# Kernel optimization log

Measured on AMD Instinct MI355X. Metric: run time of the kernel, lower is better.

## Reference

```python
import jax, jax.numpy as jnp
import numpy as np

B, C, OC, H, W = 2, 64, 128, 96, 96
HD, DI, N, R, K = C // 2, C, 16, 2, 4  # VSSBlock: hidden=C/2, d_inner=2*hidden=C, d_state, dt_rank, 4 scan dirs
EPS = 1e-5


def _conv(x, w, b, pad, groups=1):
    y = jax.lax.conv_general_dilated(x, w, (1, 1), pad, feature_group_count=groups,
                                     dimension_numbers=('NCHW', 'OIHW', 'NCHW'))
    return y + b[None, :, None, None]


def _ln(x, w, b):
    m = x.mean(-1, keepdims=True)
    v = x.var(-1, keepdims=True)
    return (x - m) * jax.lax.rsqrt(v + EPS) * w + b


def _selective_scan(xs, dts, Bs, Cs, A, D):
    # xs, dts: (B,K,DI,L); Bs, Cs: (B,K,N,L); A: (K,DI,N); D: (K,DI)
    dts = jax.nn.softplus(dts)

    def step(h, inp):
        u_t, dt_t, B_t, C_t = inp
        dA = jnp.exp(dt_t[..., None] * A)                         # (B,K,DI,N)
        h = dA * h + (dt_t * u_t)[..., None] * B_t[:, :, None, :]
        return h, jnp.einsum('bkdn,bkn->bkd', h, C_t)

    seq = (jnp.moveaxis(xs, -1, 0), jnp.moveaxis(dts, -1, 0),
           jnp.moveaxis(Bs, -1, 0), jnp.moveaxis(Cs, -1, 0))
    h0 = jnp.zeros(xs.shape[:3] + (A.shape[-1],), xs.dtype)
    _, ys = jax.lax.scan(step, h0, seq)
    return jnp.moveaxis(ys, 0, -1) + D[None, :, :, None] * xs


def _vss_block(x, ln_w, ln_b, in_w, conv_w, conv_b, xproj_w, dtproj_w, dtproj_b,
               A_logs, Ds, on_w, on_b, out_w):
    # x: (B,H,W,HD); VMamba SS2D with 4-direction cross-scan + residual
    b, hh, ww, _ = x.shape
    L = hh * ww
    h = _ln(x, ln_w, ln_b)
    xz = h @ in_w                                   # (B,H,W,2*DI)
    xp, z = jnp.split(xz, 2, axis=-1)
    xc = jnp.transpose(xp, (0, 3, 1, 2))            # (B,DI,H,W)
    xc = jax.nn.silu(_conv(xc, conv_w, conv_b, ((1, 1), (1, 1)), groups=DI))
    x_flat = xc.reshape(b, DI, L)
    x_wh = jnp.transpose(xc, (0, 1, 3, 2)).reshape(b, DI, L)
    x2 = jnp.stack([x_flat, x_wh], axis=1)
    xs = jnp.concatenate([x2, jnp.flip(x2, -1)], axis=1)      # (B,4,DI,L)
    x_dbl = jnp.einsum('bkdl,kcd->bkcl', xs, xproj_w)
    dts, Bs, Cs = jnp.split(x_dbl, [R, R + N], axis=2)
    dts = jnp.einsum('bkrl,kdr->bkdl', dts, dtproj_w) + dtproj_b[None, :, :, None]
    A = -jnp.exp(A_logs)
    ys = _selective_scan(xs, dts, Bs, Cs, A, Ds)              # (B,4,DI,L)
    inv = jnp.flip(ys[:, 2:4], -1)
    unwh = lambda t: jnp.transpose(t.reshape(b, DI, ww, hh), (0, 1, 3, 2)).reshape(b, DI, L)
    y = ys[:, 0] + inv[:, 0] + unwh(ys[:, 1]) + unwh(inv[:, 1])
    y = jnp.transpose(y.reshape(b, DI, hh, ww), (0, 2, 3, 1))
    y = _ln(y, on_w, on_b) * jax.nn.silu(z)
    return x + y @ out_w


def _forward(x, ms_dw33_w, ms_dw33_b, ms_in_w, ms_in_b, ms_scale,
             vss_ln_w, vss_ln_b, vss_in_w, vss_conv_w, vss_conv_b, vss_xproj_w,
             vss_dtproj_w, vss_dtproj_b, vss_A_logs, vss_Ds, vss_on_w, vss_on_b, vss_out_w,
             ma_conv_w, ma_conv_b, adw_h_w, adw_h_b, adw_w_w, adw_w_b,
             pw_w, pw_b, bn_w, bn_b, bn_mean, bn_var):
    vss = (vss_ln_w, vss_ln_b, vss_in_w, vss_conv_w, vss_conv_b, vss_xproj_w,
           vss_dtproj_w, vss_dtproj_b, vss_A_logs, vss_Ds, vss_on_w, vss_on_b, vss_out_w)
    # --- MambaSplit (shared VSSBlock applied to both channel halves) ---
    xd = _conv(x, ms_dw33_w, ms_dw33_b, ((1, 1), (1, 1)), groups=C)
    x1, x2 = jnp.split(xd, 2, axis=1)

    def branch(xp):
        y = _vss_block(jnp.transpose(xp, (0, 2, 3, 1)), *vss)
        return ms_scale * xp + jnp.transpose(y, (0, 3, 1, 2))

    xm = jnp.concatenate([branch(x1), branch(x2)], axis=1)
    m = xm.mean((2, 3), keepdims=True)
    v = xm.var((2, 3), keepdims=True)
    xm = (xm - m) * jax.lax.rsqrt(v + EPS) * ms_in_w[None, :, None, None] + ms_in_b[None, :, None, None]
    xm = jax.nn.leaky_relu(xm, 0.01)
    # --- MaxAvg (global avg+max pool -> 3x3 conv on 1x1 map -> sigmoid gate) ---
    pooled = jnp.concatenate([x.mean((2, 3), keepdims=True), x.max((2, 3), keepdims=True)], axis=1)
    gate = jax.nn.sigmoid(_conv(pooled, ma_conv_w, ma_conv_b, ((1, 1), (1, 1))))
    xs_ = xm + gate * x
    # --- AxialDW ---
    xs_ = xs_ + _conv(xs_, adw_h_w, adw_h_b, ((1, 1), (0, 0)), groups=C) \
              + _conv(xs_, adw_w_w, adw_w_b, ((0, 0), (1, 1)), groups=C)
    # --- BN (eval) + ReLU, 1x1 conv, 2x2 maxpool ---
    skip = jax.nn.relu((xs_ - bn_mean[None, :, None, None]) * jax.lax.rsqrt(bn_var[None, :, None, None] + EPS)
                       * bn_w[None, :, None, None] + bn_b[None, :, None, None])
    out = _conv(skip, pw_w, pw_b, ((0, 0), (0, 0)))
    down = jax.lax.reduce_window(out, -jnp.inf, jax.lax.max, (1, 1, 2, 2), (1, 1, 2, 2), 'VALID')
    return down, skip


def setup_inputs() -> dict:
    key = jax.random.key(0)
    ks = jax.random.split(key, 16)
    r = lambda i, shape, s=0.02: jax.random.normal(ks[i], shape, jnp.float32) * s
    return {
        'x': jax.random.normal(ks[0], (B, C, H, W), jnp.float32),
        'ms_dw33_w': r(1, (C, 1, 3, 3), 0.1), 'ms_dw33_b': jnp.zeros(C),
        'ms_in_w': jnp.ones(C), 'ms_in_b': jnp.zeros(C),
        'ms_scale': jnp.ones((1,)),
        'vss_ln_w': jnp.ones(HD), 'vss_ln_b': jnp.zeros(HD),
        'vss_in_w': r(2, (HD, 2 * DI)),
        'vss_conv_w': r(3, (DI, 1, 3, 3), 0.1), 'vss_conv_b': jnp.zeros(DI),
        'vss_xproj_w': r(4, (K, R + 2 * N, DI)),
        'vss_dtproj_w': r(5, (K, DI, R), 0.1), 'vss_dtproj_b': r(6, (K, DI), 0.1),
        'vss_A_logs': jnp.tile(jnp.log(jnp.arange(1, N + 1, dtype=jnp.float32)), (K, DI, 1)),
        'vss_Ds': jnp.ones((K, DI)),
        'vss_on_w': jnp.ones(DI), 'vss_on_b': jnp.zeros(DI),
        'vss_out_w': r(7, (DI, HD)),
        'ma_conv_w': r(8, (C, 2 * C, 3, 3), 0.05), 'ma_conv_b': jnp.zeros(C),
        'adw_h_w': r(9, (C, 1, 3, 1), 0.1), 'adw_h_b': jnp.zeros(C),
        'adw_w_w': r(10, (C, 1, 1, 3), 0.1), 'adw_w_b': jnp.zeros(C),
        'pw_w': r(11, (OC, C, 1, 1)), 'pw_b': jnp.zeros(OC),
        'bn_w': jnp.ones(C), 'bn_b': jnp.zeros(C),
        'bn_mean': jnp.zeros(C), 'bn_var': jnp.ones(C),
    }


def reference(x, ms_dw33_w, ms_dw33_b, ms_in_w, ms_in_b, ms_scale,
              vss_ln_w, vss_ln_b, vss_in_w, vss_conv_w, vss_conv_b, vss_xproj_w,
              vss_dtproj_w, vss_dtproj_b, vss_A_logs, vss_Ds, vss_on_w, vss_on_b, vss_out_w,
              ma_conv_w, ma_conv_b, adw_h_w, adw_h_b, adw_w_w, adw_w_b,
              pw_w, pw_b, bn_w, bn_b, bn_mean, bn_var):
    return _forward(x, ms_dw33_w, ms_dw33_b, ms_in_w, ms_in_b, ms_scale,
                    vss_ln_w, vss_ln_b, vss_in_w, vss_conv_w, vss_conv_b, vss_xproj_w,
                    vss_dtproj_w, vss_dtproj_b, vss_A_logs, vss_Ds, vss_on_w, vss_on_b, vss_out_w,
                    ma_conv_w, ma_conv_b, adw_h_w, adw_h_b, adw_w_w, adw_w_b,
                    pw_w, pw_b, bn_w, bn_b, bn_mean, bn_var)
```

## Files before the change

kernel.cpp:

```cpp
#include <hip/hip_runtime.h>
#include <hip/hip_bf16.h>

typedef __hip_bfloat16 bf16;
#define DEV __device__ __forceinline__

constexpr int B_ = 2, C_ = 64, H_ = 96, W_ = 96, L_ = 9216;
constexpr int HD_ = 32, DI_ = 64, N_ = 16, K_ = 4, BB_ = 4;
constexpr int OC_ = 128;
constexpr int CH_ = 384, CL_ = 24;
constexpr float EPSF = 1e-5f;
constexpr int DOWN_SZ = B_ * OC_ * 48 * 48;

typedef __attribute__((ext_vector_type(8))) short short8;
typedef __attribute__((ext_vector_type(4))) float f32x4;

DEV float softplusf(float x) { return x > 15.f ? x : __logf(1.f + __expf(x)); }
DEV float b2f(bf16 v) { return __bfloat162float(v); }
DEV float lo16f(unsigned v) { return __uint_as_float(v << 16); }
DEV float hi16f(unsigned v) { return __uint_as_float(v & 0xffff0000u); }
DEV void unpk(uint4 a, uint4 b, float* v) {
  v[0] = lo16f(a.x); v[1] = hi16f(a.x); v[2] = lo16f(a.y); v[3] = hi16f(a.y);
  v[4] = lo16f(a.z); v[5] = hi16f(a.z); v[6] = lo16f(a.w); v[7] = hi16f(a.w);
  v[8] = lo16f(b.x); v[9] = hi16f(b.x); v[10] = lo16f(b.y); v[11] = hi16f(b.y);
  v[12] = lo16f(b.z); v[13] = hi16f(b.z); v[14] = lo16f(b.w); v[15] = hi16f(b.w);
}

__constant__ float kLogN[16] = {
  0.0f, 0.69314718f, 1.09861229f, 1.38629436f, 1.60943791f, 1.79175947f,
  1.94591015f, 2.07944154f, 2.19722458f, 2.30258509f, 2.39789527f,
  2.48490665f, 2.56494936f, 2.63905733f, 2.70805020f, 2.77258872f};

DEV void chunk_addr(int k, int chunk, int& idx0, int& stride) {
  int r4 = chunk & 3, q = chunk >> 2;
  if (k == 0)      { idx0 = chunk * CL_;                        stride = 1;   }
  else if (k == 1) { idx0 = (24 * r4) * 96 + q;                 stride = 96;  }
  else if (k == 2) { idx0 = L_ - 1 - chunk * CL_;               stride = -1;  }
  else             { idx0 = (95 - 24 * r4) * 96 + (95 - q);     stride = -96; }
}

DEV void pow_tree(float e1, float* ep) {
  float e2 = e1 * e1, e4 = e2 * e2, e8 = e4 * e4;
  float e3 = e2 * e1, e5 = e4 * e1, e6 = e4 * e2, e7 = e4 * e3;
  ep[0] = e1;  ep[1] = e2;  ep[2] = e3;  ep[3] = e4;
  ep[4] = e5;  ep[5] = e6;  ep[6] = e7;  ep[7] = e8;
  ep[8] = e8 * e1;  ep[9] = e8 * e2;  ep[10] = e8 * e3;  ep[11] = e8 * e4;
  ep[12] = e8 * e5; ep[13] = e8 * e6; ep[14] = e8 * e7;  ep[15] = e8 * e8;
}

DEV void ldrow(const float* __restrict__ bB, const bf16* __restrict__ bC,
               const bf16* __restrict__ xcb, int d, int idx,
               uint4& qb0, uint4& qb1, uint4& qc0, uint4& qc1,
               float& t0, float& t1, float& u) {
  int uix = __builtin_amdgcn_readfirstlane(idx);
  const float* p = bB + (size_t)uix * 12;
  qb0 = *(const uint4*)p; qb1 = *(const uint4*)(p + 4);
  t0 = p[8]; t1 = p[9];
  const uint4* cq = (const uint4*)(bC + (size_t)uix * 16);
  qc0 = cq[0]; qc1 = cq[1];
  u = b2f(xcb[(size_t)idx * DI_ + d]);
}

DEV void pstep(uint4 qb0, uint4 qb1, uint4 qc0, uint4 qc1, float t0, float t1, float u,
               float w0, float w1, float bia, float A1, float Dk,
               float* h, float& S, float& yout) {
  float Bv[16], Cv[16];
  unpk(qb0, qb1, Bv); unpk(qc0, qc1, Cv);
  float dt = softplusf(fmaf(t0, w0, fmaf(t1, w1, bia)));
  S += dt;
  float du = dt * u;
  float ep[16];
  pow_tree(__expf(dt * A1), ep);
  float m[16];
#pragma unroll
  for (int n = 0; n < N_; n++) {
    h[n] = fmaf(ep[n], h[n], du * Bv[n]);
    m[n] = h[n] * Cv[n];
  }
  float a0 = m[0] + m[1], a1 = m[2] + m[3], a2 = m[4] + m[5], a3 = m[6] + m[7];
  float a4 = m[8] + m[9], a5 = m[10] + m[11], a6 = m[12] + m[13], a7 = m[14] + m[15];
  float b0 = a0 + a1, b1 = a2 + a3, b2 = a4 + a5, b3 = a6 + a7;
  yout = fmaf(Dk, u, (b0 + b1) + (b2 + b3));
}

__global__ void k_dw33(const float* __restrict__ x, const float* __restrict__ w,
                       const float* __restrict__ bias, float* __restrict__ out) {
  int t = blockIdx.x * 256 + threadIdx.x;
  if (t >= B_ * C_ * L_) return;
  int wi = t % W_, hi = (t / W_) % H_, c = (t / L_) % C_;
  float acc = bias[c];
#pragma unroll
  for (int dy = -1; dy <= 1; dy++) {
    int hh = hi + dy; if (hh < 0 || hh >= H_) continue;
#pragma unroll
    for (int dx = -1; dx <= 1; dx++) {
      int ww = wi + dx; if (ww < 0 || ww >= W_) continue;
      acc = fmaf(x[t + dy * W_ + dx], w[c * 9 + (dy + 1) * 3 + (dx + 1)], acc);
    }
  }
  out[t] = acc;
}

__global__ __launch_bounds__(256, 4) void k_ln_inproj(
    const float* __restrict__ xd, const float* __restrict__ lnw,
    const float* __restrict__ lnb, const float* __restrict__ inw,
    float* __restrict__ xzA, bf16* __restrict__ xzBh) {
  int bb = blockIdx.y, t = threadIdx.x;
  int b = bb & 1, co = (bb >> 1) * HD_;
  int idx0 = blockIdx.x * 64;
  __shared__ float xds[32 * 68];
  __shared__ float meanA[64], rstdA[64];
  int lane = t & 63;
  for (int r = 0; r < 8; r++) {
    int c = r * 4 + (t >> 6);
    xds[c * 68 + lane] = xd[(size_t)(b * C_ + co + c) * L_ + idx0 + lane];
  }
  __syncthreads();
  if (t < 64) {
    float s = 0.f, sq = 0.f;
#pragma unroll
    for (int c = 0; c < 32; c++) { float v = xds[c * 68 + t]; s += v; sq = fmaf(v, v, sq); }
    float mean = s * (1.f / HD_);
    float var = sq * (1.f / HD_) - mean * mean;
    meanA[t] = mean; rstdA[t] = rsqrtf(var + EPSF);
  }
  __syncthreads();
  for (int i = t; i < 2048; i += 256) {
    int c = i >> 6, idx = i & 63;
    float v = xds[c * 68 + idx];
    xds[c * 68 + idx] = (v - meanA[idx]) * rstdA[idx] * lnw[c] + lnb[c];
  }
  __syncthreads();
  int oc = t & 127, g = t >> 7;
  float acc[32];
#pragma unroll
  for (int j = 0; j < 32; j++) acc[j] = 0.f;
  for (int c = 0; c < 32; c++) {
    float wv = inw[c * 128 + oc];
    const float4* row = reinterpret_cast<const float4*>(&xds[c * 68 + g * 32]);
#pragma unroll
    for (int j4 = 0; j4 < 8; j4++) {
      float4 xv = row[j4];
      acc[j4 * 4 + 0] = fmaf(xv.x, wv, acc[j4 * 4 + 0]);
      acc[j4 * 4 + 1] = fmaf(xv.y, wv, acc[j4 * 4 + 1]);
      acc[j4 * 4 + 2] = fmaf(xv.z, wv, acc[j4 * 4 + 2]);
      acc[j4 * 4 + 3] = fmaf(xv.w, wv, acc[j4 * 4 + 3]);
    }
  }
  int occ = oc & 63;
  if (oc < 64) {
#pragma unroll
    for (int j = 0; j < 32; j++)
      xzA[(size_t)(bb * L_ + idx0 + g * 32 + j) * 64 + occ] = acc[j];
  } else {
#pragma unroll
    for (int j = 0; j < 32; j++)
      xzBh[(size_t)(bb * L_ + idx0 + g * 32 + j) * 64 + occ] = __float2bfloat16(acc[j]);
  }
}

__global__ void k_dwsilu(const float* __restrict__ xzA, const float* __restrict__ cw,
                         const float* __restrict__ cb, bf16* __restrict__ xch) {
  int t = blockIdx.x * 256 + threadIdx.x;
  int d = t & 63, idx = (t >> 6) % L_, bb = t / (L_ * DI_);
  int wi = idx % W_, hi = idx / W_;
  float acc = cb[d];
#pragma unroll
  for (int dy = -1; dy <= 1; dy++) {
    int hh = hi + dy; if (hh < 0 || hh >= H_) continue;
#pragma unroll
    for (int dx = -1; dx <= 1; dx++) {
      int ww = wi + dx; if (ww < 0 || ww >= W_) continue;
      acc = fmaf(xzA[(size_t)(bb * L_ + hh * W_ + ww) * 64 + d],
                 cw[d * 9 + (dy + 1) * 3 + (dx + 1)], acc);
    }
  }
  acc = acc / (1.f + __expf(-acc));
  xch[t] = __float2bfloat16(acc);
}

__global__ void k_wprep(const float* __restrict__ xpw, const float* __restrict__ alog,
                        bf16* __restrict__ wh, float* __restrict__ aux) {
  int i = blockIdx.x * 256 + threadIdx.x;
  if (i < 144 * 64) {
    int n = i >> 6;
    wh[i] = __float2bfloat16(n < 136 ? xpw[i] : 0.f);
  }
  if (blockIdx.x == 0 && threadIdx.x < 256) {
    int kd = threadIdx.x;
    const float* al = alog + kd * N_;
    float a0 = al[0];
    bool lin = true;
#pragma unroll
    for (int n = 1; n < N_; n++) lin = lin && (fabsf(al[n] - a0 - kLogN[n]) < 3e-5f);
    aux[kd] = -__expf(a0);
    aux[256 + kd] = lin ? 1.f : 0.f;
#pragma unroll
    for (int n = 0; n < N_; n++) aux[512 + kd * N_ + n] = -__expf(al[n]);
  }
}

__global__ __launch_bounds__(256, 4) void k_xdbl_mfma(
    const bf16* __restrict__ xch, const bf16* __restrict__ wh,
    float* __restrict__ xdblB, bf16* __restrict__ xdblC) {
  int w = threadIdx.x >> 6, lane = threadIdx.x & 63;
  int bb = blockIdx.y;
  int mtile = blockIdx.x * 4 + w;
  int idx0 = mtile * 16;
  int m = lane & 15, quad = lane >> 4;
  const bf16* arow = xch + ((size_t)bb * L_ + idx0 + m) * 64 + quad * 8;
  short8 a0 = *reinterpret_cast<const short8*>(arow);
  short8 a1 = *reinterpret_cast<const short8*>(arow + 32);
#pragma unroll
  for (int nt = 0; nt < 9; nt++) {
    int n = nt * 16 + m;
    const bf16* brow = wh + n * 64 + quad * 8;
    short8 b0 = *reinterpret_cast<const short8*>(brow);
    short8 b1 = *reinterpret_cast<const short8*>(brow + 32);
    f32x4 acc = {0.f, 0.f, 0.f, 0.f};
    acc = __builtin_amdgcn_mfma_f32_16x16x32_bf16(a0, b0, acc, 0, 0, 0);
    acc = __builtin_amdgcn_mfma_f32_16x16x32_bf16(a1, b1, acc, 0, 0, 0);
    if (n < 136) {
      int k4 = (n >= 102) ? 3 : (n >= 68) ? 2 : (n >= 34) ? 1 : 0;
      int c = n - k4 * 34;
      size_t row = (size_t)(bb * K_ + k4) * L_ + idx0 + quad * 4;
      if (c < 2) {
        float* db = xdblB + row * 12 + 8 + c;
        db[0] = acc[0]; db[12] = acc[1]; db[24] = acc[2]; db[36] = acc[3];
      } else if (c < 18) {
        bf16* bp = (bf16*)(xdblB + row * 12) + (c - 2);
        bp[0] = __float2bfloat16(acc[0]);  bp[24] = __float2bfloat16(acc[1]);
        bp[48] = __float2bfloat16(acc[2]); bp[72] = __float2bfloat16(acc[3]);
      } else {
        bf16* cp = xdblC + row * 16 + (c - 18);
        cp[0] = __float2bfloat16(acc[0]);  cp[16] = __float2bfloat16(acc[1]);
        cp[32] = __float2bfloat16(acc[2]); cp[48] = __float2bfloat16(acc[3]);
      }
    }
  }
}

__global__ __launch_bounds__(256, 4) void k_scan1(
    const float* __restrict__ xdblB, const bf16* __restrict__ xdblC,
    const bf16* __restrict__ xch, const float* __restrict__ dtw,
    const float* __restrict__ dtb, const float* __restrict__ Dsw,
    const float* __restrict__ aux, bf16* __restrict__ hbuf,
    float* __restrict__ ssum, bf16* __restrict__ ylocal, bf16* __restrict__ cdt) {
  int w = threadIdx.x >> 6, d = threadIdx.x & 63;
  int chunk = blockIdx.x * 4 + w, k = blockIdx.y, bb = blockIdx.z;
  float w0 = dtw[(k * DI_ + d) * 2 + 0], w1 = dtw[(k * DI_ + d) * 2 + 1];
  float bia = dtb[k * DI_ + d];
  float Dk = Dsw[k * DI_ + d];
  float A1 = aux[k * 64 + d];
  bool chain = (__ballot(aux[256 + k * 64 + d] > 0.5f) == ~0ull);
  float h[N_];
#pragma unroll
  for (int n = 0; n < N_; n++) h[n] = 0.f;
  int idx0, stride;
  chunk_addr(k, chunk, idx0, stride);
  const float* bB = xdblB + (size_t)(bb * K_ + k) * L_ * 12;
  const bf16* bC = xdblC + (size_t)(bb * K_ + k) * L_ * 16;
  const bf16* xcb = xch + (size_t)bb * L_ * DI_;
  bf16* yb = ylocal + (size_t)(bb * K_ + k) * L_ * DI_;
  bf16* cb2 = cdt + (size_t)(bb * K_ + k) * L_ * DI_;
  float S = 0.f;
  if (chain) {
    uint4 qb0a, qb1a, qc0a, qc1a; float t0a, t1a, ua;
    uint4 qb0b, qb1b, qc0b, qc1b; float t0b, t1b, ub;
    int ia = idx0;
    ldrow(bB, bC, xcb, d, ia, qb0a, qb1a, qc0a, qc1a, t0a, t1a, ua);
    for (int s = 0; s < CL_; s += 2) {
      int ib = ia + stride;
      ldrow(bB, bC, xcb, d, ib, qb0b, qb1b, qc0b, qc1b, t0b, t1b, ub);
      float y;
      pstep(qb0a, qb1a, qc0a, qc1a, t0a, t1a, ua, w0, w1, bia, A1, Dk, h, S, y);
      yb[(size_t)ia * DI_ + d] = __float2bfloat16(y);
      cb2[(size_t)ia * DI_ + d] = __float2bfloat16(S);
      int in2 = (s + 2 < CL_) ? ib + stride : idx0;
      ldrow(bB, bC, xcb, d, in2, qb0a, qb1a, qc0a, qc1a, t0a, t1a, ua);
      pstep(qb0b, qb1b, qc0b, qc1b, t0b, t1b, ub, w0, w1, bia, A1, Dk, h, S, y);
      yb[(size_t)ib * DI_ + d] = __float2bfloat16(y);
      cb2[(size_t)ib * DI_ + d] = __float2bfloat16(S);
      ia = in2;
    }
  } else {
    float A[N_];
#pragma unroll
    for (int n = 0; n < N_; n++) A[n] = aux[512 + (k * 64 + d) * N_ + n];
    int idx = idx0;
    for (int s = 0; s < CL_; s++) {
      uint4 qb0, qb1, qc0, qc1; float t0, t1, u;
      ldrow(bB, bC, xcb, d, idx, qb0, qb1, qc0, qc1, t0, t1, u);
      float Bv[16], Cv[16];
      unpk(qb0, qb1, Bv); unpk(qc0, qc1, Cv);
      float dt = softplusf(fmaf(t0, w0, fmaf(t1, w1, bia)));
      S += dt;
      float du = dt * u;
      float y = 0.f;
#pragma unroll
      for (int n = 0; n < N_; n++) {
        h[n] = fmaf(__expf(dt * A[n]), h[n], du * Bv[n]);
        y = fmaf(h[n], Cv[n], y);
      }
      y = fmaf(Dk, u, y);
      yb[(size_t)idx * DI_ + d] = __float2bfloat16(y);
      cb2[(size_t)idx * DI_ + d] = __float2bfloat16(S);
      idx += stride;
    }
  }
  size_t base = (size_t)((bb * K_ + k) * CH_ + chunk) * DI_ + d;
  ssum[base] = S;
#pragma unroll
  for (int n = 0; n < N_; n++) hbuf[base * N_ + n] = __float2bfloat16(h[n]);
}

__global__ void k_scan2(const float* __restrict__ aux, const float* __restrict__ ssum,
                        bf16* __restrict__ hbuf) {
  int t = blockIdx.x * 256 + threadIdx.x;
  int n = t & 15, d = (t >> 4) & 63, kk = (t >> 10) & 3, bb = t >> 12;
  float A = aux[512 + (kk * 64 + d) * N_ + n];
  size_t row = (size_t)(bb * K_ + kk) * CH_ * DI_ + d;
  constexpr int U = 16;
  float Sb[U], hb[U];
#pragma unroll
  for (int j = 0; j < U; j++) {
    size_t sb = row + (size_t)j * DI_;
    Sb[j] = ssum[sb]; hb[j] = b2f(hbuf[sb * N_ + n]);
  }
  float hp = 0.f;
  for (int c = 0; c < CH_; c += U) {
    float S2[U], h2[U];
    if (c + U < CH_) {
#pragma unroll
      for (int j = 0; j < U; j++) {
        size_t sb = row + (size_t)(c + U + j) * DI_;
        S2[j] = ssum[sb]; h2[j] = b2f(hbuf[sb * N_ + n]);
      }
    } else {
#pragma unroll
      for (int j = 0; j < U; j++) { S2[j] = 0.f; h2[j] = 0.f; }
    }
#pragma unroll
    for (int j = 0; j < U; j++) {
      size_t sb = row + (size_t)(c + j) * DI_;
      float e = __expf(A * Sb[j]);
      hbuf[sb * N_ + n] = __float2bfloat16(hp);
      hp = fmaf(e, hp, hb[j]);
    }
#pragma unroll
    for (int j = 0; j < U; j++) { Sb[j] = S2[j]; hb[j] = h2[j]; }
  }
}

__global__ __launch_bounds__(256, 4) void k_combine(
    const bf16* __restrict__ ylocal, const bf16* __restrict__ cdt,
    const bf16* __restrict__ hbuf, const bf16* __restrict__ xdblC,
    const float* __restrict__ aux, const bf16* __restrict__ xzBh,
    const float* __restrict__ xd, const float* __restrict__ onw,
    const float* __restrict__ onb, const float* __restrict__ outw,
    const float* __restrict__ mssc, float* __restrict__ xm) {
  int w = threadIdx.x >> 6, d = threadIdx.x & 63;
  int idx = blockIdx.x * 4 + w, bb = blockIdx.y;
  int b = bb & 1, co = (bb >> 1) * HD_;
  int hii = idx / 96, wii = idx - hii * 96;
  int lt = wii * 96 + hii;
  int lk[4] = { idx, lt, L_ - 1 - idx, L_ - 1 - lt };
  float y = 0.f;
#pragma unroll
  for (int k = 0; k < K_; k++) {
    int chunk = lk[k] / CL_;
    size_t row = (size_t)(bb * K_ + k) * L_ + idx;
    float yk = b2f(ylocal[row * DI_ + d]);
    float S = b2f(cdt[row * DI_ + d]);
    float A1 = aux[k * 64 + d];
    bool chain = (__ballot(aux[256 + k * 64 + d] > 0.5f) == ~0ull);
    const bf16* hb = hbuf + ((size_t)((bb * K_ + k) * CH_ + chunk) * DI_ + d) * N_;
    uint4 qh0 = *(const uint4*)hb, qh1 = *(const uint4*)(hb + 8);
    float hv[16];
    unpk(qh0, qh1, hv);
    const uint4* cq = (const uint4*)(xdblC + row * 16);
    float Cv[16];
    unpk(cq[0], cq[1], Cv);
    float corr;
    if (chain) {
      float ep[16];
      pow_tree(__expf(A1 * S), ep);
      float m[16];
#pragma unroll
      for (int n = 0; n < N_; n++) m[n] = Cv[n] * (ep[n] * hv[n]);
      float a0 = m[0] + m[1], a1 = m[2] + m[3], a2 = m[4] + m[5], a3 = m[6] + m[7];
      float a4 = m[8] + m[9], a5 = m[10] + m[11], a6 = m[12] + m[13], a7 = m[14] + m[15];
      corr = ((a0 + a1) + (a2 + a3)) + ((a4 + a5) + (a6 + a7));
    } else {
      corr = 0.f;
#pragma unroll
      for (int n = 0; n < N_; n++) {
        float A = aux[512 + (k * 64 + d) * N_ + n];
        corr = fmaf(Cv[n] * hv[n], __expf(A * S), corr);
      }
    }
    y += yk + corr;
  }
  float s = y, sq = y * y;
#pragma unroll
  for (int m = 1; m < 64; m <<= 1) { s += __shfl_xor(s, m, 64); sq += __shfl_xor(sq, m, 64); }
  float mean = s * (1.f / DI_);
  float var = sq * (1.f / DI_) - mean * mean;
  float rstd = rsqrtf(var + EPSF);
  float yn = (y - mean) * rstd * onw[d] + onb[d];
  float z = b2f(xzBh[(size_t)(bb * L_ + idx) * 64 + d]);
  float g = yn * (z / (1.f + __expf(-z)));
  __shared__ float gs[4][DI_];
  gs[w][d] = g;
  __syncthreads();
  if (d < HD_) {
    float acc = 0.f;
#pragma unroll
    for (int dd = 0; dd < DI_; dd++) acc = fmaf(gs[w][dd], outw[dd * HD_ + d], acc);
    size_t xi = (size_t)(b * C_ + co + d) * L_ + idx;
    float xp = xd[xi];
    xm[xi] = mssc[0] * xp + xp + acc;
  }
}

__global__ __launch_bounds__(1024) void k_stats(
    const float* __restrict__ xm, const float* __restrict__ x,
    float* __restrict__ inm, float* __restrict__ inr,
    float* __restrict__ xmean, float* __restrict__ xmax) {
  int bc = blockIdx.x, t = threadIdx.x;
  const float* pm = xm + (size_t)bc * L_;
  const float* px = x + (size_t)bc * L_;
  float s = 0.f, sq = 0.f, xs = 0.f, mx = -1e30f;
  for (int i = t; i < L_; i += 1024) {
    float v = pm[i]; s += v; sq = fmaf(v, v, sq);
    float xv = px[i]; xs += xv; mx = fmaxf(mx, xv);
  }
  __shared__ float red[64];
#pragma unroll
  for (int m = 1; m < 64; m <<= 1) {
    s += __shfl_xor(s, m, 64); sq += __shfl_xor(sq, m, 64);
    xs += __shfl_xor(xs, m, 64); mx = fmaxf(mx, __shfl_xor(mx, m, 64));
  }
  int wid = t >> 6;
  if ((t & 63) == 0) { red[wid] = s; red[16 + wid] = sq; red[32 + wid] = xs; red[48 + wid] = mx; }
  __syncthreads();
  if (t == 0) {
    s = 0.f; sq = 0.f; xs = 0.f; mx = -1e30f;
#pragma unroll
    for (int i = 0; i < 16; i++) {
      s += red[i]; sq += red[16 + i]; xs += red[32 + i]; mx = fmaxf(mx, red[48 + i]);
    }
    float mean = s * (1.f / L_);
    float var = sq * (1.f / L_) - mean * mean;
    inm[bc] = mean;
    inr[bc] = rsqrtf(var + EPSF);
    xmean[bc] = xs * (1.f / L_);
    xmax[bc] = mx;
  }
}

__global__ void k_xs(const float* __restrict__ xm, const float* __restrict__ inm,
                     const float* __restrict__ inr, const float* __restrict__ msw,
                     const float* __restrict__ msb, const float* __restrict__ xmean,
                     const float* __restrict__ xmax, const float* __restrict__ maw,
                     const float* __restrict__ mab, const float* __restrict__ x,
                     float* __restrict__ xs2) {
  int t = blockIdx.x * 256 + threadIdx.x;
  int bc = t / L_, c = bc & 63, b = bc >> 6;
  __shared__ float gsh;
  if (threadIdx.x < 64) {
    int ic = threadIdx.x;
    float p = xmean[b * 64 + ic] * maw[(c * 128 + ic) * 9 + 4]
            + xmax[b * 64 + ic] * maw[(c * 128 + 64 + ic) * 9 + 4];
#pragma unroll
    for (int m = 1; m < 64; m <<= 1) p += __shfl_xor(p, m, 64);
    if (ic == 0) gsh = 1.f / (1.f + __expf(-(p + mab[c])));
  }
  __syncthreads();
  float gate = gsh;
  float v = xm[t];
  v = (v - inm[bc]) * inr[bc] * msw[c] + msb[c];
  v = v > 0.f ? v : 0.01f * v;
  xs2[t] = v + gate * x[t];
}

__global__ void k_axbn(const float* __restrict__ xs2, const float* __restrict__ hw,
                       const float* __restrict__ hb, const float* __restrict__ wwt,
                       const float* __restrict__ wb, const float* __restrict__ bnw,
                       const float* __restrict__ bnb, const float* __restrict__ bnm,
                       const float* __restrict__ bnv, float* __restrict__ skipo) {
  int t = blockIdx.x * 256 + threadIdx.x;
  if (t >= B_ * C_ * L_) return;
  int wi = t % W_, hi = (t / W_) % H_, c = (t / L_) % C_;
  float a = xs2[t];
  float hacc = hb[c];
#pragma unroll
  for (int dy = -1; dy <= 1; dy++) {
    int hh = hi + dy; if (hh < 0 || hh >= H_) continue;
    hacc = fmaf(xs2[t + dy * W_], hw[c * 3 + dy + 1], hacc);
  }
  float wacc = wb[c];
#pragma unroll
  for (int dx = -1; dx <= 1; dx++) {
    int ww = wi + dx; if (ww < 0 || ww >= W_) continue;
    wacc = fmaf(xs2[t + dx], wwt[c * 3 + dx + 1], wacc);
  }
  float v = a + hacc + wacc;
  float sv = (v - bnm[c]) * rsqrtf(bnv[c] + EPSF) * bnw[c] + bnb[c];
  skipo[t] = fmaxf(sv, 0.f);
}

__global__ void k_pwpool(const float* __restrict__ skipo, const float* __restrict__ pww,
                         const float* __restrict__ pwb, float* __restrict__ down) {
  int h2 = blockIdx.x, b = blockIdx.y, t = threadIdx.x;
  int oc0 = blockIdx.z * 32;
  __shared__ float sk[64 * 192];
  for (int i = t; i < 64 * 192; i += 256) {
    int c = i / 192, rw = i % 192, r = rw / 96, wcol = rw % 96;
    sk[i] = skipo[((size_t)(b * C_ + c) * H_ + (2 * h2 + r)) * W_ + wcol];
  }
  __syncthreads();
  for (int o = t; o < 32 * 48; o += 256) {
    int oc = oc0 + o / 48, w2 = o % 48;
    float s0 = 0.f, s1 = 0.f, s2 = 0.f, s3 = 0.f;
#pragma unroll 8
    for (int c = 0; c < 64; c++) {
      float wv = pww[oc * 64 + c];
      const float* sp = &sk[c * 192 + 2 * w2];
      s0 = fmaf(sp[0], wv, s0);
      s1 = fmaf(sp[1], wv, s1);
      s2 = fmaf(sp[96], wv, s2);
      s3 = fmaf(sp[97], wv, s3);
    }
    float v = fmaxf(fmaxf(s0, s1), fmaxf(s2, s3)) + pwb[oc];
    down[((size_t)(b * OC_ + oc) * 48 + h2) * 48 + w2] = v;
  }
}

extern "C" void kernel_launch(void* const* d_in, const int* in_sizes, int n_in,
                              void* d_out, int out_size, void* d_ws, size_t ws_size,
                              hipStream_t stream) {
  const float* x     = (const float*)d_in[0];
  const float* dw33w = (const float*)d_in[1];
  const float* dw33b = (const float*)d_in[2];
  const float* msw   = (const float*)d_in[3];
  const float* msb   = (const float*)d_in[4];
  const float* mssc  = (const float*)d_in[5];
  const float* lnw   = (const float*)d_in[6];
  const float* lnb   = (const float*)d_in[7];
  const float* inw   = (const float*)d_in[8];
  const float* cw    = (const float*)d_in[9];
  const float* cb    = (const float*)d_in[10];
  const float* xpw   = (const float*)d_in[11];
  const float* dtw   = (const float*)d_in[12];
  const float* dtb   = (const float*)d_in[13];
  const float* alog  = (const float*)d_in[14];
  const float* Dsw   = (const float*)d_in[15];
  const float* onw   = (const float*)d_in[16];
  const float* onb   = (const float*)d_in[17];
  const float* outw  = (const float*)d_in[18];
  const float* maw   = (const float*)d_in[19];
  const float* mab   = (const float*)d_in[20];
  const float* ahw   = (const float*)d_in[21];
  const float* ahb   = (const float*)d_in[22];
  const float* aww   = (const float*)d_in[23];
  const float* awb   = (const float*)d_in[24];
  const float* pww   = (const float*)d_in[25];
  const float* pwb   = (const float*)d_in[26];
  const float* bnw   = (const float*)d_in[27];
  const float* bnb   = (const float*)d_in[28];
  const float* bnm   = (const float*)d_in[29];
  const float* bnv   = (const float*)d_in[30];

  float* ws = (float*)d_ws;
  float* xd    = ws;
  float* xzA   = xd + 1179648;
  bf16*  hbuf  = (bf16*)xzA;
  bf16*  xzBh  = (bf16*)(xzA + 3145728);
  float* xdblB = xzA + 3145728 + 1179648;
  bf16*  xdblC = (bf16*)(xdblB + 1769472);
  float* ssum  = xdblB + 1769472 + 1179648;
  bf16*  ylocal = (bf16*)(ssum + 393216);
  bf16*  cdt   = (bf16*)(ssum + 393216 + 4718592);
  float* xmR   = ssum + 393216 + 4718592 + 4718592;
  bf16*  xch   = (bf16*)xmR;
  float* xm    = xmR;
  float* xs2   = (float*)ylocal;
  float* st    = xmR + 1179648;
  float* inm = st, *inr = st + 128, *xmean = st + 256, *xmaxv = st + 384;
  float* aux   = st + 512;
  bf16*  wh    = (bf16*)(aux + 4608);

  float* outp = (float*)d_out;
  float* down = outp;
  float* skipo = outp + DOWN_SZ;

  dim3 b256(256);
  int nEl = B_ * C_ * L_;

  k_wprep<<<dim3(36), b256, 0, stream>>>(xpw, alog, wh, aux);
  k_dw33<<<dim3((nEl + 255) / 256), b256, 0, stream>>>(x, dw33w, dw33b, xd);
  k_ln_inproj<<<dim3(L_ / 64, BB_), b256, 0, stream>>>(xd, lnw, lnb, inw, xzA, xzBh);
  k_dwsilu<<<dim3(BB_ * L_ * DI_ / 256), b256, 0, stream>>>(xzA, cw, cb, xch);
  k_xdbl_mfma<<<dim3(L_ / 64, BB_), b256, 0, stream>>>(xch, wh, xdblB, xdblC);
  k_scan1<<<dim3(CH_ / 4, K_, BB_), b256, 0, stream>>>(xdblB, xdblC, xch, dtw, dtb, Dsw,
                                                       aux, hbuf, ssum, ylocal, cdt);
  k_scan2<<<dim3(BB_ * K_ * DI_ * N_ / 256), b256, 0, stream>>>(aux, ssum, hbuf);
  k_combine<<<dim3(L_ / 4, BB_), b256, 0, stream>>>(ylocal, cdt, hbuf, xdblC, aux, xzBh,
                                                    xd, onw, onb, outw, mssc, xm);
  k_stats<<<dim3(B_ * C_), dim3(1024), 0, stream>>>(xm, x, inm, inr, xmean, xmaxv);
  k_xs<<<dim3((nEl + 255) / 256), b256, 0, stream>>>(xm, inm, inr, msw, msb, xmean, xmaxv, maw, mab, x, xs2);
  k_axbn<<<dim3((nEl + 255) / 256), b256, 0, stream>>>(xs2, ahw, ahb, aww, awb, bnw, bnb, bnm, bnv, skipo);
  k_pwpool<<<dim3(48, B_, 4), b256, 0, stream>>>(skipo, pww, pwb, down);
}
```

Measured before the change: 333.0 us.

## Restructure chunked scan into three passes with carried-in states and halved chunk length

Replaces the two-pass chunked scan plus correction-in-combine with a three-pass scheme. Pass one computes only per-chunk end states and dt sums, pass two propagates chunk prefixes, and pass three re-runs each chunk from its true initial state to produce final outputs. The combine kernel then just sums the four directions. This drops the cumulative-dt buffer and the per-element correction work, and the chunk length is halved to 12 to double parallelism. The cost is reading B, u and dt twice, a longer sequential prefix pass over 768 chunks, and a larger state buffer.

```diff
diff --git a/kernel.cpp b/kernel.cpp
--- a/kernel.cpp
+++ b/kernel.cpp
@@ -7,7 +7,7 @@
 constexpr int B_ = 2, C_ = 64, H_ = 96, W_ = 96, L_ = 9216;
 constexpr int HD_ = 32, DI_ = 64, N_ = 16, K_ = 4, BB_ = 4;
 constexpr int OC_ = 128;
-constexpr int CH_ = 384, CL_ = 24;
+constexpr int CH_ = 768, CL_ = 12;
 constexpr float EPSF = 1e-5f;
 constexpr int DOWN_SZ = B_ * OC_ * 48 * 48;
 
@@ -31,11 +31,11 @@
   2.48490665f, 2.56494936f, 2.63905733f, 2.70805020f, 2.77258872f};
 
 DEV void chunk_addr(int k, int chunk, int& idx0, int& stride) {
-  int r4 = chunk & 3, q = chunk >> 2;
+  int r8 = chunk & 7, q = chunk >> 3;
   if (k == 0)      { idx0 = chunk * CL_;                        stride = 1;   }
-  else if (k == 1) { idx0 = (24 * r4) * 96 + q;                 stride = 96;  }
+  else if (k == 1) { idx0 = (12 * r8) * 96 + q;                 stride = 96;  }
   else if (k == 2) { idx0 = L_ - 1 - chunk * CL_;               stride = -1;  }
-  else             { idx0 = (95 - 24 * r4) * 96 + (95 - q);     stride = -96; }
+  else             { idx0 = (95 - 12 * r8) * 96 + (95 - q);     stride = -96; }
 }
 
 DEV void pow_tree(float e1, float* ep) {
@@ -47,10 +47,18 @@
   ep[12] = e8 * e5; ep[13] = e8 * e6; ep[14] = e8 * e7;  ep[15] = e8 * e8;
 }
 
-DEV void ldrow(const float* __restrict__ bB, const bf16* __restrict__ bC,
-               const bf16* __restrict__ xcb, int d, int idx,
-               uint4& qb0, uint4& qb1, uint4& qc0, uint4& qc1,
-               float& t0, float& t1, float& u) {
+DEV void ld_bu(const float* __restrict__ bB, const bf16* __restrict__ xcb, int d, int idx,
+               uint4& qb0, uint4& qb1, float& t0, float& t1, float& u) {
+  int uix = __builtin_amdgcn_readfirstlane(idx);
+  const float* p = bB + (size_t)uix * 12;
+  qb0 = *(const uint4*)p; qb1 = *(const uint4*)(p + 4);
+  t0 = p[8]; t1 = p[9];
+  u = b2f(xcb[(size_t)idx * DI_ + d]);
+}
+DEV void ld_bcu(const float* __restrict__ bB, const bf16* __restrict__ bC,
+                const bf16* __restrict__ xcb, int d, int idx,
+                uint4& qb0, uint4& qb1, uint4& qc0, uint4& qc1,
+                float& t0, float& t1, float& u) {
   int uix = __builtin_amdgcn_readfirstlane(idx);
   const float* p = bB + (size_t)uix * 12;
   qb0 = *(const uint4*)p; qb1 = *(const uint4*)(p + 4);
@@ -58,28 +66,6 @@
   const uint4* cq = (const uint4*)(bC + (size_t)uix * 16);
   qc0 = cq[0]; qc1 = cq[1];
   u = b2f(xcb[(size_t)idx * DI_ + d]);
-}
-
-DEV void pstep(uint4 qb0, uint4 qb1, uint4 qc0, uint4 qc1, float t0, float t1, float u,
-               float w0, float w1, float bia, float A1, float Dk,
-               float* h, float& S, float& yout) {
-  float Bv[16], Cv[16];
-  unpk(qb0, qb1, Bv); unpk(qc0, qc1, Cv);
-  float dt = softplusf(fmaf(t0, w0, fmaf(t1, w1, bia)));
-  S += dt;
-  float du = dt * u;
-  float ep[16];
-  pow_tree(__expf(dt * A1), ep);
-  float m[16];
-#pragma unroll
-  for (int n = 0; n < N_; n++) {
-    h[n] = fmaf(ep[n], h[n], du * Bv[n]);
-    m[n] = h[n] * Cv[n];
-  }
-  float a0 = m[0] + m[1], a1 = m[2] + m[3], a2 = m[4] + m[5], a3 = m[6] + m[7];
-  float a4 = m[8] + m[9], a5 = m[10] + m[11], a6 = m[12] + m[13], a7 = m[14] + m[15];
-  float b0 = a0 + a1, b1 = a2 + a3, b2 = a4 + a5, b3 = a6 + a7;
-  yout = fmaf(Dk, u, (b0 + b1) + (b2 + b3));
 }
 
 __global__ void k_dw33(const float* __restrict__ x, const float* __restrict__ w,
@@ -240,11 +226,109 @@
 }
 
 __global__ __launch_bounds__(256, 4) void k_scan1(
+    const float* __restrict__ xdblB, const bf16* __restrict__ xch,
+    const float* __restrict__ dtw, const float* __restrict__ dtb,
+    const float* __restrict__ aux, bf16* __restrict__ hbuf,
+    float* __restrict__ ssum) {
+  int w = threadIdx.x >> 6, d = threadIdx.x & 63;
+  int chunk = blockIdx.x * 4 + w, k = blockIdx.y, bb = blockIdx.z;
+  float w0 = dtw[(k * DI_ + d) * 2 + 0], w1 = dtw[(k * DI_ + d) * 2 + 1];
+  float bia = dtb[k * DI_ + d];
+  float A1 = aux[k * 64 + d];
+  bool chain = (__ballot(aux[256 + k * 64 + d] > 0.5f) == ~0ull);
+  float h[N_];
+#pragma unroll
+  for (int n = 0; n < N_; n++) h[n] = 0.f;
+  int idx0, stride;
+  chunk_addr(k, chunk, idx0, stride);
+  const float* bB = xdblB + (size_t)(bb * K_ + k) * L_ * 12;
+  const bf16* xcb = xch + (size_t)bb * L_ * DI_;
+  float S = 0.f;
+  if (chain) {
+    int idx = idx0;
+#pragma unroll 2
+    for (int s = 0; s < CL_; s++) {
+      uint4 qb0, qb1; float t0, t1, u;
+      ld_bu(bB, xcb, d, idx, qb0, qb1, t0, t1, u);
+      float Bv[16];
+      unpk(qb0, qb1, Bv);
+      float dt = softplusf(fmaf(t0, w0, fmaf(t1, w1, bia)));
+      S += dt;
+      float du = dt * u;
+      float ep[16];
+      pow_tree(__expf(dt * A1), ep);
+#pragma unroll
+      for (int n = 0; n < N_; n++) h[n] = fmaf(ep[n], h[n], du * Bv[n]);
+      idx += stride;
+    }
+  } else {
+    float A[N_];
+#pragma unroll
+    for (int n = 0; n < N_; n++) A[n] = aux[512 + (k * 64 + d) * N_ + n];
+    int idx = idx0;
+    for (int s = 0; s < CL_; s++) {
+      uint4 qb0, qb1; float t0, t1, u;
+      ld_bu(bB, xcb, d, idx, qb0, qb1, t0, t1, u);
+      float Bv[16];
+      unpk(qb0, qb1, Bv);
+      float dt = softplusf(fmaf(t0, w0, fmaf(t1, w1, bia)));
+      S += dt;
+      float du = dt * u;
+#pragma unroll
+      for (int n = 0; n < N_; n++) h[n] = fmaf(__expf(dt * A[n]), h[n], du * Bv[n]);
+      idx += stride;
+    }
+  }
+  size_t base = (size_t)((bb * K_ + k) * CH_ + chunk) * DI_ + d;
+  ssum[base] = S;
+#pragma unroll
+  for (int n = 0; n < N_; n++) hbuf[base * N_ + n] = __float2bfloat16(h[n]);
+}
+
+__global__ void k_scan2(const float* __restrict__ aux, const float* __restrict__ ssum,
+                        bf16* __restrict__ hbuf) {
+  int t = blockIdx.x * 256 + threadIdx.x;
+  int n = t & 15, d = (t >> 4) & 63, kk = (t >> 10) & 3, bb = t >> 12;
+  float A = aux[512 + (kk * 64 + d) * N_ + n];
+  size_t row = (size_t)(bb * K_ + kk) * CH_ * DI_ + d;
+  constexpr int U = 16;
+  float Sb[U], hb[U];
+#pragma unroll
+  for (int j = 0; j < U; j++) {
+    size_t sb = row + (size_t)j * DI_;
+    Sb[j] = ssum[sb]; hb[j] = b2f(hbuf[sb * N_ + n]);
+  }
+  float hp = 0.f;
+  for (int c = 0; c < CH_; c += U) {
+    float S2[U], h2[U];
+    if (c + U < CH_) {
+#pragma unroll
+      for (int j = 0; j < U; j++) {
+        size_t sb = row + (size_t)(c + U + j) * DI_;
+        S2[j] = ssum[sb]; h2[j] = b2f(hbuf[sb * N_ + n]);
+      }
+    } else {
+#pragma unroll
+      for (int j = 0; j < U; j++) { S2[j] = 0.f; h2[j] = 0.f; }
+    }
+#pragma unroll
+    for (int j = 0; j < U; j++) {
+      size_t sb = row + (size_t)(c + j) * DI_;
+      float e = __expf(A * Sb[j]);
+      hbuf[sb * N_ + n] = __float2bfloat16(hp);
+      hp = fmaf(e, hp, hb[j]);
+    }
+#pragma unroll
+    for (int j = 0; j < U; j++) { Sb[j] = S2[j]; hb[j] = h2[j]; }
+  }
+}
+
+__global__ __launch_bounds__(256, 4) void k_scan3(
     const float* __restrict__ xdblB, const bf16* __restrict__ xdblC,
     const bf16* __restrict__ xch, const float* __restrict__ dtw,
     const float* __restrict__ dtb, const float* __restrict__ Dsw,
-    const float* __restrict__ aux, bf16* __restrict__ hbuf,
-    float* __restrict__ ssum, bf16* __restrict__ ylocal, bf16* __restrict__ cdt) {
+    const float* __restrict__ aux, const bf16* __restrict__ hbuf,
+    bf16* __restrict__ ydir) {
   int w = threadIdx.x >> 6, d = threadIdx.x & 63;
   int chunk = blockIdx.x * 4 + w, k = blockIdx.y, bb = blockIdx.z;
   float w0 = dtw[(k * DI_ + d) * 2 + 0], w1 = dtw[(k * DI_ + d) * 2 + 1];
@@ -253,34 +337,42 @@
   float A1 = aux[k * 64 + d];
   bool chain = (__ballot(aux[256 + k * 64 + d] > 0.5f) == ~0ull);
   float h[N_];
-#pragma unroll
-  for (int n = 0; n < N_; n++) h[n] = 0.f;
+  size_t base = (size_t)((bb * K_ + k) * CH_ + chunk) * DI_ + d;
+  {
+    const bf16* hb = hbuf + base * N_;
+    uint4 qh0 = *(const uint4*)hb, qh1 = *(const uint4*)(hb + 8);
+    unpk(qh0, qh1, h);
+  }
   int idx0, stride;
   chunk_addr(k, chunk, idx0, stride);
   const float* bB = xdblB + (size_t)(bb * K_ + k) * L_ * 12;
   const bf16* bC = xdblC + (size_t)(bb * K_ + k) * L_ * 16;
   const bf16* xcb = xch + (size_t)bb * L_ * DI_;
-  bf16* yb = ylocal + (size_t)(bb * K_ + k) * L_ * DI_;
-  bf16* cb2 = cdt + (size_t)(bb * K_ + k) * L_ * DI_;
-  float S = 0.f;
+  bf16* yb = ydir + (size_t)(bb * K_ + k) * L_ * DI_;
   if (chain) {
-    uint4 qb0a, qb1a, qc0a, qc1a; float t0a, t1a, ua;
-    uint4 qb0b, qb1b, qc0b, qc1b; float t0b, t1b, ub;
-    int ia = idx0;
-    ldrow(bB, bC, xcb, d, ia, qb0a, qb1a, qc0a, qc1a, t0a, t1a, ua);
-    for (int s = 0; s < CL_; s += 2) {
-      int ib = ia + stride;
-      ldrow(bB, bC, xcb, d, ib, qb0b, qb1b, qc0b, qc1b, t0b, t1b, ub);
-      float y;
-      pstep(qb0a, qb1a, qc0a, qc1a, t0a, t1a, ua, w0, w1, bia, A1, Dk, h, S, y);
-      yb[(size_t)ia * DI_ + d] = __float2bfloat16(y);
-      cb2[(size_t)ia * DI_ + d] = __float2bfloat16(S);
-      int in2 = (s + 2 < CL_) ? ib + stride : idx0;
-      ldrow(bB, bC, xcb, d, in2, qb0a, qb1a, qc0a, qc1a, t0a, t1a, ua);
-      pstep(qb0b, qb1b, qc0b, qc1b, t0b, t1b, ub, w0, w1, bia, A1, Dk, h, S, y);
-      yb[(size_t)ib * DI_ + d] = __float2bfloat16(y);
-      cb2[(size_t)ib * DI_ + d] = __float2bfloat16(S);
-      ia = in2;
+    int idx = idx0;
+#pragma unroll 2
+    for (int s = 0; s < CL_; s++) {
+      uint4 qb0, qb1, qc0, qc1; float t0, t1, u;
+      ld_bcu(bB, bC, xcb, d, idx, qb0, qb1, qc0, qc1, t0, t1, u);
+      float Bv[16], Cv[16];
+      unpk(qb0, qb1, Bv); unpk(qc0, qc1, Cv);
+      float dt = softplusf(fmaf(t0, w0, fmaf(t1, w1, bia)));
+      float du = dt * u;
+      float ep[16];
+      pow_tree(__expf(dt * A1), ep);
+      float m[16];
+#pragma unroll
+      for (int n = 0; n < N_; n++) {
+        h[n] = fmaf(ep[n], h[n], du * Bv[n]);
+        m[n] = h[n] * Cv[n];
+      }
+      float a0 = m[0] + m[1], a1 = m[2] + m[3], a2 = m[4] + m[5], a3 = m[6] + m[7];
+      float a4 = m[8] + m[9], a5 = m[10] + m[11], a6 = m[12] + m[13], a7 = m[14] + m[15];
+      float b0 = a0 + a1, b1 = a2 + a3, b2 = a4 + a5, b3 = a6 + a7;
+      float y = fmaf(Dk, u, (b0 + b1) + (b2 + b3));
+      yb[(size_t)idx * DI_ + d] = __float2bfloat16(y);
+      idx += stride;
     }
   } else {
     float A[N_];
@@ -289,11 +381,10 @@
     int idx = idx0;
     for (int s = 0; s < CL_; s++) {
       uint4 qb0, qb1, qc0, qc1; float t0, t1, u;
-      ldrow(bB, bC, xcb, d, idx, qb0, qb1, qc0, qc1, t0, t1, u);
+      ld_bcu(bB, bC, xcb, d, idx, qb0, qb1, qc0, qc1, t0, t1, u);
       float Bv[16], Cv[16];
       unpk(qb0, qb1, Bv); unpk(qc0, qc1, Cv);
       float dt = softplusf(fmaf(t0, w0, fmaf(t1, w1, bia)));
-      S += dt;
       float du = dt * u;
       float y = 0.f;
 #pragma unroll
@@ -303,103 +394,22 @@
       }
       y = fmaf(Dk, u, y);
       yb[(size_t)idx * DI_ + d] = __float2bfloat16(y);
-      cb2[(size_t)idx * DI_ + d] = __float2bfloat16(S);
       idx += stride;
     }
   }
-  size_t base = (size_t)((bb * K_ + k) * CH_ + chunk) * DI_ + d;
-  ssum[base] = S;
-#pragma unroll
-  for (int n = 0; n < N_; n++) hbuf[base * N_ + n] = __float2bfloat16(h[n]);
-}
-
-__global__ void k_scan2(const float* __restrict__ aux, const float* __restrict__ ssum,
-                        bf16* __restrict__ hbuf) {
-  int t = blockIdx.x * 256 + threadIdx.x;
-  int n = t & 15, d = (t >> 4) & 63, kk = (t >> 10) & 3, bb = t >> 12;
-  float A = aux[512 + (kk * 64 + d) * N_ + n];
-  size_t row = (size_t)(bb * K_ + kk) * CH_ * DI_ + d;
-  constexpr int U = 16;
-  float Sb[U], hb[U];
-#pragma unroll
-  for (int j = 0; j < U; j++) {
-    size_t sb = row + (size_t)j * DI_;
-    Sb[j] = ssum[sb]; hb[j] = b2f(hbuf[sb * N_ + n]);
-  }
-  float hp = 0.f;
-  for (int c = 0; c < CH_; c += U) {
-    float S2[U], h2[U];
-    if (c + U < CH_) {
-#pragma unroll
-      for (int j = 0; j < U; j++) {
-        size_t sb = row + (size_t)(c + U + j) * DI_;
-        S2[j] = ssum[sb]; h2[j] = b2f(hbuf[sb * N_ + n]);
-      }
-    } else {
-#pragma unroll
-      for (int j = 0; j < U; j++) { S2[j] = 0.f; h2[j] = 0.f; }
-    }
-#pragma unroll
-    for (int j = 0; j < U; j++) {
-      size_t sb = row + (size_t)(c + j) * DI_;
-      float e = __expf(A * Sb[j]);
-      hbuf[sb * N_ + n] = __float2bfloat16(hp);
-      hp = fmaf(e, hp, hb[j]);
-    }
-#pragma unroll
-    for (int j = 0; j < U; j++) { Sb[j] = S2[j]; hb[j] = h2[j]; }
-  }
-}
-
-__global__ __launch_bounds__(256, 4) void k_combine(
-    const bf16* __restrict__ ylocal, const bf16* __restrict__ cdt,
-    const bf16* __restrict__ hbuf, const bf16* __restrict__ xdblC,
-    const float* __restrict__ aux, const bf16* __restrict__ xzBh,
-    const float* __restrict__ xd, const float* __restrict__ onw,
-    const float* __restrict__ onb, const float* __restrict__ outw,
-    const float* __restrict__ mssc, float* __restrict__ xm) {
+}
+
+__global__ void k_combine(const bf16* __restrict__ ydir, const bf16* __restrict__ xzBh,
+                          const float* __restrict__ xd, const float* __restrict__ onw,
+                          const float* __restrict__ onb, const float* __restrict__ outw,
+                          const float* __restrict__ mssc, float* __restrict__ xm) {
   int w = threadIdx.x >> 6, d = threadIdx.x & 63;
   int idx = blockIdx.x * 4 + w, bb = blockIdx.y;
   int b = bb & 1, co = (bb >> 1) * HD_;
-  int hii = idx / 96, wii = idx - hii * 96;
-  int lt = wii * 96 + hii;
-  int lk[4] = { idx, lt, L_ - 1 - idx, L_ - 1 - lt };
-  float y = 0.f;
-#pragma unroll
-  for (int k = 0; k < K_; k++) {
-    int chunk = lk[k] / CL_;
-    size_t row = (size_t)(bb * K_ + k) * L_ + idx;
-    float yk = b2f(ylocal[row * DI_ + d]);
-    float S = b2f(cdt[row * DI_ + d]);
-    float A1 = aux[k * 64 + d];
-    bool chain = (__ballot(aux[256 + k * 64 + d] > 0.5f) == ~0ull);
-    const bf16* hb = hbuf + ((size_t)((bb * K_ + k) * CH_ + chunk) * DI_ + d) * N_;
-    uint4 qh0 = *(const uint4*)hb, qh1 = *(const uint4*)(hb + 8);
-    float hv[16];
-    unpk(qh0, qh1, hv);
-    const uint4* cq = (const uint4*)(xdblC + row * 16);
-    float Cv[16];
-    unpk(cq[0], cq[1], Cv);
-    float corr;
-    if (chain) {
-      float ep[16];
-      pow_tree(__expf(A1 * S), ep);
-      float m[16];
-#pragma unroll
-      for (int n = 0; n < N_; n++) m[n] = Cv[n] * (ep[n] * hv[n]);
-      float a0 = m[0] + m[1], a1 = m[2] + m[3], a2 = m[4] + m[5], a3 = m[6] + m[7];
-      float a4 = m[8] + m[9], a5 = m[10] + m[11], a6 = m[12] + m[13], a7 = m[14] + m[15];
-      corr = ((a0 + a1) + (a2 + a3)) + ((a4 + a5) + (a6 + a7));
-    } else {
-      corr = 0.f;
-#pragma unroll
-      for (int n = 0; n < N_; n++) {
-        float A = aux[512 + (k * 64 + d) * N_ + n];
-        corr = fmaf(Cv[n] * hv[n], __expf(A * S), corr);
-      }
-    }
-    y += yk + corr;
-  }
+  const bf16* yd = ydir + (size_t)bb * K_ * L_ * DI_;
+  size_t off = (size_t)idx * DI_ + d;
+  float y = b2f(yd[off]) + b2f(yd[(size_t)L_ * DI_ + off])
+          + b2f(yd[(size_t)2 * L_ * DI_ + off]) + b2f(yd[(size_t)3 * L_ * DI_ + off]);
   float s = y, sq = y * y;
 #pragma unroll
   for (int m = 1; m < 64; m <<= 1) { s += __shfl_xor(s, m, 64); sq += __shfl_xor(sq, m, 64); }
@@ -573,18 +583,18 @@
 
   float* ws = (float*)d_ws;
   float* xd    = ws;
-  float* xzA   = xd + 1179648;
-  bf16*  hbuf  = (bf16*)xzA;
-  bf16*  xzBh  = (bf16*)(xzA + 3145728);
-  float* xdblB = xzA + 3145728 + 1179648;
+  float* hreg  = xd + 1179648;
+  bf16*  hbuf  = (bf16*)hreg;
+  float* xzA   = hreg;
+  bf16*  xzBh  = (bf16*)(hreg + 6291456);
+  float* xdblB = hreg + 6291456 + 1179648;
   bf16*  xdblC = (bf16*)(xdblB + 1769472);
   float* ssum  = xdblB + 1769472 + 1179648;
-  bf16*  ylocal = (bf16*)(ssum + 393216);
-  bf16*  cdt   = (bf16*)(ssum + 393216 + 4718592);
-  float* xmR   = ssum + 393216 + 4718592 + 4718592;
+  bf16*  ydir  = (bf16*)(ssum + 786432);
+  float* xmR   = ssum + 786432 + 4718592;
   bf16*  xch   = (bf16*)xmR;
   float* xm    = xmR;
-  float* xs2   = (float*)ylocal;
+  float* xs2   = (float*)ydir;
   float* st    = xmR + 1179648;
   float* inm = st, *inr = st + 128, *xmean = st + 256, *xmaxv = st + 384;
   float* aux   = st + 512;
@@ -602,11 +612,11 @@
   k_ln_inproj<<<dim3(L_ / 64, BB_), b256, 0, stream>>>(xd, lnw, lnb, inw, xzA, xzBh);
   k_dwsilu<<<dim3(BB_ * L_ * DI_ / 256), b256, 0, stream>>>(xzA, cw, cb, xch);
   k_xdbl_mfma<<<dim3(L_ / 64, BB_), b256, 0, stream>>>(xch, wh, xdblB, xdblC);
-  k_scan1<<<dim3(CH_ / 4, K_, BB_), b256, 0, stream>>>(xdblB, xdblC, xch, dtw, dtb, Dsw,
-                                                       aux, hbuf, ssum, ylocal, cdt);
+  k_scan1<<<dim3(CH_ / 4, K_, BB_), b256, 0, stream>>>(xdblB, xch, dtw, dtb, aux, hbuf, ssum);
   k_scan2<<<dim3(BB_ * K_ * DI_ * N_ / 256), b256, 0, stream>>>(aux, ssum, hbuf);
-  k_combine<<<dim3(L_ / 4, BB_), b256, 0, stream>>>(ylocal, cdt, hbuf, xdblC, aux, xzBh,
-                                                    xd, onw, onb, outw, mssc, xm);
+  k_scan3<<<dim3(CH_ / 4, K_, BB_), b256, 0, stream>>>(xdblB, xdblC, xch, dtw, dtb, Dsw,
+                                                      aux, hbuf, ydir);
+  k_combine<<<dim3(L_ / 4, BB_), b256, 0, stream>>>(ydir, xzBh, xd, onw, onb, outw, mssc, xm);
   k_stats<<<dim3(B_ * C_), dim3(1024), 0, stream>>>(xm, x, inm, inr, xmean, xmaxv);
   k_xs<<<dim3((nEl + 255) / 256), b256, 0, stream>>>(xm, inm, inr, msw, msb, xmean, xmaxv, maw, mab, x, xs2);
   k_axbn<<<dim3((nEl + 255) / 256), b256, 0, stream>>>(xs2, ahw, ahb, aww, awb, bnw, bnb, bnm, bnv, skipo);
```

Result: slower. 344.4 us (+3.4%).
